# Performance work log

Measured on AMD Instinct MI355X. Metric: run time of the kernel, lower is better.

The kernel has to match this reference:

```python
import jax, jax.numpy as jnp
from jax import lax
import numpy as np

B, T, D, U = 32, 2048, 512, 512


def setup_inputs() -> dict:
    key = jax.random.key(0)
    k1, k2, k3 = jax.random.split(key, 3)
    x = jax.random.normal(k1, (B, T, D), dtype=jnp.float32)
    # keras 'uniform' initializer ~ U(-0.05, 0.05)
    kernel = jax.random.uniform(k2, (D, U), dtype=jnp.float32, minval=-0.05, maxval=0.05)
    recurrent_kernel = jax.random.uniform(k3, (U, U), dtype=jnp.float32, minval=-0.05, maxval=0.05)
    return {"x": x, "kernel": kernel, "recurrent_kernel": recurrent_kernel}


def reference(x, kernel, recurrent_kernel):
    # Linear RNN: h_t = x_t @ W + h_{t-1} @ U, h_0 = 0 (keras RNN default zero state).
    # Precompute the input projection as one big GEMM (same math, batched once).
    xk = jnp.einsum('btd,du->btu', x, kernel)  # [B, T, U]

    def step(h, xt):
        h = xt + h @ recurrent_kernel
        return h, h

    h0 = jnp.zeros((x.shape[0], recurrent_kernel.shape[0]), dtype=x.dtype)
    _, ys = lax.scan(step, h0, jnp.swapaxes(xk, 0, 1))  # ys: [T, B, U]
    return jnp.swapaxes(ys, 0, 1)  # [B, T, U] (return_sequences=True semantics)
```

## Files before the change

kernel.cpp:

```cpp
#include <hip/hip_runtime.h>
#include <hip/hip_bf16.h>


#define B_ 32
#define T_ 2048
#define D_ 512
#define U_ 512
#define C_ 8
#define P_ 256

typedef unsigned short u16;
typedef __attribute__((ext_vector_type(8))) short bf16x8;
typedef __attribute__((ext_vector_type(4))) float f32x4;

__device__ __forceinline__ float bf2f(u16 h) {
    union { unsigned u; float f; } v; v.u = ((unsigned)h) << 16; return v.f;
}
__device__ __forceinline__ u16 f2bf(float f) {
    union { float f; unsigned u; } v; v.f = f;
    unsigned x = v.u;
    unsigned r = x + 0x7fffu + ((x >> 16) & 1u);
    return (u16)(r >> 16);
}

__global__ void prep_kernel(const float* __restrict__ W, const float* __restrict__ R,
                            u16* __restrict__ Wt, u16* __restrict__ Rt, u16* __restrict__ Rb) {
    int idx = blockIdx.x * blockDim.x + threadIdx.x;
    int r = idx >> 9, c = idx & 511;
    float w = W[idx];
    float rv = R[idx];
    Wt[c * 512 + r] = f2bf(w);
    Rt[c * 512 + r] = f2bf(rv);
    Rb[idx] = f2bf(rv);
}

__global__ __launch_bounds__(256, 3) void gemmA_kernel(const float* __restrict__ x,
        const u16* __restrict__ Wt, u16* __restrict__ xk) {
    int bid = blockIdx.x;
    int mg = bid >> 2, ng = bid & 3;
    int m0 = mg * 128, n0 = ng * 128;
    int w = threadIdx.x >> 6, l = threadIdx.x & 63;
    int wm = (w >> 1) * 64, wn = (w & 1) * 64;
    int lane_m = l & 15, quad = l >> 4;

    f32x4 acc[4][4];
#pragma unroll
    for (int i = 0; i < 4; i++)
#pragma unroll
        for (int j = 0; j < 4; j++) acc[i][j] = (f32x4){0.f, 0.f, 0.f, 0.f};

    const float* xbase = x + (size_t)(m0 + wm + lane_m) * D_ + quad * 8;
    const u16* wbase = Wt + (size_t)(n0 + wn + lane_m) * D_ + quad * 8;

    for (int kk = 0; kk < 16; kk++) {
        bf16x8 af[4], bf[4];
#pragma unroll
        for (int mi = 0; mi < 4; mi++) {
            const float* p = xbase + (size_t)mi * 16 * D_ + kk * 32;
            float4 lo = *(const float4*)p;
            float4 hi = *(const float4*)(p + 4);
            bf16x8 t;
            t[0] = (short)f2bf(lo.x); t[1] = (short)f2bf(lo.y);
            t[2] = (short)f2bf(lo.z); t[3] = (short)f2bf(lo.w);
            t[4] = (short)f2bf(hi.x); t[5] = (short)f2bf(hi.y);
            t[6] = (short)f2bf(hi.z); t[7] = (short)f2bf(hi.w);
            af[mi] = t;
        }
#pragma unroll
        for (int ni = 0; ni < 4; ni++)
            bf[ni] = *(const bf16x8*)(wbase + (size_t)ni * 16 * D_ + kk * 32);
#pragma unroll
        for (int mi = 0; mi < 4; mi++)
#pragma unroll
            for (int ni = 0; ni < 4; ni++)
                acc[mi][ni] = __builtin_amdgcn_mfma_f32_16x16x32_bf16(af[mi], bf[ni], acc[mi][ni], 0, 0, 0);
    }
#pragma unroll
    for (int mi = 0; mi < 4; mi++)
#pragma unroll
        for (int ni = 0; ni < 4; ni++) {
            int col = n0 + wn + ni * 16 + lane_m;
#pragma unroll
            for (int i = 0; i < 4; i++) {
                int row = m0 + wm + mi * 16 + quad * 4 + i;
                xk[(size_t)row * U_ + col] = f2bf(acc[mi][ni][i]);
            }
        }
}

__global__ __launch_bounds__(512, 2) void pass1_kernel(
        const u16* __restrict__ xk, const u16* __restrict__ Rt,
        float* __restrict__ Lc,
        float* __restrict__ Eout) {
    __shared__ u16 H[B_][U_ + 8];
    int k = blockIdx.x;
    int t0 = k * C_;
    int tid = threadIdx.x;
    int w = tid >> 6, l = tid & 63;
    int lane_m = l & 15, quad = l >> 4;
    int wn = w * 64;

    for (int idx = tid; idx < B_ * U_; idx += 512) {
        int b = idx >> 9, u = idx & 511;
        H[b][u] = 0;
    }
    __syncthreads();

    f32x4 acc[2][4];
    for (int t = t0; t < t0 + C_; t++) {
#pragma unroll
        for (int mi = 0; mi < 2; mi++)
#pragma unroll
            for (int ni = 0; ni < 4; ni++) {
                int u = wn + ni * 16 + lane_m;
#pragma unroll
                for (int i = 0; i < 4; i++) {
                    int b = mi * 16 + quad * 4 + i;
                    acc[mi][ni][i] = bf2f(xk[((size_t)b * T_ + t) * U_ + u]);
                }
            }
        for (int kk = 0; kk < 16; kk++) {
            bf16x8 a0 = *(const bf16x8*)&H[lane_m][kk * 32 + quad * 8];
            bf16x8 a1 = *(const bf16x8*)&H[16 + lane_m][kk * 32 + quad * 8];
#pragma unroll
            for (int ni = 0; ni < 4; ni++) {
                bf16x8 b = *(const bf16x8*)(Rt + (size_t)(wn + ni * 16 + lane_m) * U_ + kk * 32 + quad * 8);
                acc[0][ni] = __builtin_amdgcn_mfma_f32_16x16x32_bf16(a0, b, acc[0][ni], 0, 0, 0);
                acc[1][ni] = __builtin_amdgcn_mfma_f32_16x16x32_bf16(a1, b, acc[1][ni], 0, 0, 0);
            }
        }
        __syncthreads();
#pragma unroll
        for (int mi = 0; mi < 2; mi++)
#pragma unroll
            for (int ni = 0; ni < 4; ni++) {
                int u = wn + ni * 16 + lane_m;
#pragma unroll
                for (int i = 0; i < 4; i++) {
                    int b = mi * 16 + quad * 4 + i;
                    float v = acc[mi][ni][i];
                    H[b][u] = f2bf(v);
                    Lc[((size_t)t * B_ + b) * U_ + u] = v;
                }
            }
        __syncthreads();
    }
#pragma unroll
    for (int mi = 0; mi < 2; mi++)
#pragma unroll
        for (int ni = 0; ni < 4; ni++) {
            int u = wn + ni * 16 + lane_m;
#pragma unroll
            for (int i = 0; i < 4; i++) {
                int b = mi * 16 + quad * 4 + i;
                Eout[((size_t)k * B_ + b) * U_ + u] = acc[mi][ni][i];
            }
        }
}

__global__ __launch_bounds__(512, 2) void ks_kernel(const float* __restrict__ Esrc,
        float* __restrict__ Edst, const u16* __restrict__ Mt, int d) {
    int k = blockIdx.x;
    int tid = threadIdx.x, w = tid >> 6, l = tid & 63;
    if (k < d) {
        const float4* s = (const float4*)(Esrc + (size_t)k * B_ * U_);
        float4* dst = (float4*)(Edst + (size_t)k * B_ * U_);
        for (int i = tid; i < B_ * U_ / 4; i += 512) dst[i] = s[i];
        return;
    }
    int lane_m = l & 15, quad = l >> 4, wn = w * 64;
    const float* Ek = Esrc + (size_t)k * B_ * U_;
    const float* Ep = Esrc + (size_t)(k - d) * B_ * U_;
    f32x4 acc[2][4];
#pragma unroll
    for (int mi = 0; mi < 2; mi++)
#pragma unroll
        for (int ni = 0; ni < 4; ni++) {
            int u = wn + ni * 16 + lane_m;
#pragma unroll
            for (int i = 0; i < 4; i++) {
                int b = mi * 16 + quad * 4 + i;
                acc[mi][ni][i] = Ek[(size_t)b * U_ + u];
            }
        }
    for (int kk = 0; kk < 16; kk++) {
        bf16x8 a[2];
#pragma unroll
        for (int mi = 0; mi < 2; mi++) {
            const float* p = Ep + (size_t)(mi * 16 + lane_m) * U_ + kk * 32 + quad * 8;
            float4 lo = *(const float4*)p;
            float4 hi = *(const float4*)(p + 4);
            bf16x8 t;
            t[0] = (short)f2bf(lo.x); t[1] = (short)f2bf(lo.y);
            t[2] = (short)f2bf(lo.z); t[3] = (short)f2bf(lo.w);
            t[4] = (short)f2bf(hi.x); t[5] = (short)f2bf(hi.y);
            t[6] = (short)f2bf(hi.z); t[7] = (short)f2bf(hi.w);
            a[mi] = t;
        }
#pragma unroll
        for (int ni = 0; ni < 4; ni++) {
            bf16x8 b = *(const bf16x8*)(Mt + (size_t)(wn + ni * 16 + lane_m) * U_ + kk * 32 + quad * 8);
            acc[0][ni] = __builtin_amdgcn_mfma_f32_16x16x32_bf16(a[0], b, acc[0][ni], 0, 0, 0);
            acc[1][ni] = __builtin_amdgcn_mfma_f32_16x16x32_bf16(a[1], b, acc[1][ni], 0, 0, 0);
        }
    }
#pragma unroll
    for (int mi = 0; mi < 2; mi++)
#pragma unroll
        for (int ni = 0; ni < 4; ni++) {
            int u = wn + ni * 16 + lane_m;
#pragma unroll
            for (int i = 0; i < 4; i++) {
                int b = mi * 16 + quad * 4 + i;
                Edst[(size_t)k * B_ * U_ + (size_t)b * U_ + u] = acc[mi][ni][i];
            }
        }
}

__global__ __launch_bounds__(512, 2) void carry_kernel(const float* __restrict__ Eb,
        const u16* __restrict__ Rt, u16* __restrict__ Sb, u16* __restrict__ S2) {
    int k = blockIdx.x;
    int tid = threadIdx.x, w = tid >> 6, l = tid & 63;
    if (k == P_ - 1) {
        for (int i = tid; i < B_ * U_; i += 512) { Sb[i] = 0; S2[i] = 0; }
        return;
    }
    const float* E = Eb + (size_t)k * B_ * U_;
    u16* sb = Sb + (size_t)(k + 1) * B_ * U_;
    u16* s2o = S2 + (size_t)(k + 1) * B_ * U_;
    for (int i = tid; i < B_ * U_; i += 512) sb[i] = f2bf(E[i]);

    int lane_m = l & 15, quad = l >> 4, wn = w * 64;
    f32x4 acc[2][4];
#pragma unroll
    for (int mi = 0; mi < 2; mi++)
#pragma unroll
        for (int ni = 0; ni < 4; ni++) acc[mi][ni] = (f32x4){0.f, 0.f, 0.f, 0.f};
    for (int kk = 0; kk < 16; kk++) {
        bf16x8 a[2];
#pragma unroll
        for (int mi = 0; mi < 2; mi++) {
            const float* p = E + (size_t)(mi * 16 + lane_m) * U_ + kk * 32 + quad * 8;
            float4 lo = *(const float4*)p;
            float4 hi = *(const float4*)(p + 4);
            bf16x8 t;
            t[0] = (short)f2bf(lo.x); t[1] = (short)f2bf(lo.y);
            t[2] = (short)f2bf(lo.z); t[3] = (short)f2bf(lo.w);
            t[4] = (short)f2bf(hi.x); t[5] = (short)f2bf(hi.y);
            t[6] = (short)f2bf(hi.z); t[7] = (short)f2bf(hi.w);
            a[mi] = t;
        }
#pragma unroll
        for (int ni = 0; ni < 4; ni++) {
            bf16x8 b = *(const bf16x8*)(Rt + (size_t)(wn + ni * 16 + lane_m) * U_ + kk * 32 + quad * 8);
            acc[0][ni] = __builtin_amdgcn_mfma_f32_16x16x32_bf16(a[0], b, acc[0][ni], 0, 0, 0);
            acc[1][ni] = __builtin_amdgcn_mfma_f32_16x16x32_bf16(a[1], b, acc[1][ni], 0, 0, 0);
        }
    }
#pragma unroll
    for (int mi = 0; mi < 2; mi++)
#pragma unroll
        for (int ni = 0; ni < 4; ni++) {
            int u = wn + ni * 16 + lane_m;
#pragma unroll
            for (int i = 0; i < 4; i++) {
                int b = mi * 16 + quad * 4 + i;
                s2o[(size_t)b * U_ + u] = f2bf(acc[mi][ni][i]);
            }
        }
}

__global__ __launch_bounds__(256, 2) void pass3g_kernel(
        const float* __restrict__ Lc, const u16* __restrict__ Sb,
        const u16* __restrict__ S2,
        const u16* __restrict__ P2, const u16* __restrict__ P4,
        const u16* __restrict__ P6, const u16* __restrict__ P8,
        float* __restrict__ out) {
    int bid = blockIdx.x;
    int k = bid >> 3, j = bid & 7;
    int t = k * C_ + j;
    int tid = threadIdx.x, w = tid >> 6, l = tid & 63;
    int lane_m = l & 15, quad = l >> 4;
    int wn = w * 128;

    f32x4 acc[2][8];
    const float* lc = Lc + (size_t)t * B_ * U_;
#pragma unroll
    for (int mi = 0; mi < 2; mi++)
#pragma unroll
        for (int ni = 0; ni < 8; ni++) {
            int u = wn + ni * 16 + lane_m;
#pragma unroll
            for (int i = 0; i < 4; i++) {
                int b = mi * 16 + quad * 4 + i;
                acc[mi][ni][i] = lc[(size_t)b * U_ + u];
            }
        }

    if (j == 0) {
        const u16* s2 = S2 + (size_t)k * B_ * U_;
#pragma unroll
        for (int mi = 0; mi < 2; mi++)
#pragma unroll
            for (int ni = 0; ni < 8; ni++) {
                int u = wn + ni * 16 + lane_m;
#pragma unroll
                for (int i = 0; i < 4; i++) {
                    int b = mi * 16 + quad * 4 + i;
                    acc[mi][ni][i] += bf2f(s2[(size_t)b * U_ + u]);
                }
            }
    } else {
        const u16* A = ((j & 1) ? Sb : S2) + (size_t)k * B_ * U_;
        const u16* Bm = (j & 1)
            ? ((j == 1) ? P2 : (j == 3) ? P4 : (j == 5) ? P6 : P8)
            : ((j == 2) ? P2 : (j == 4) ? P4 : P6);
        for (int kk = 0; kk < 16; kk++) {
            bf16x8 a0 = *(const bf16x8*)(A + (size_t)lane_m * U_ + kk * 32 + quad * 8);
            bf16x8 a1 = *(const bf16x8*)(A + (size_t)(16 + lane_m) * U_ + kk * 32 + quad * 8);
#pragma unroll
            for (int ni = 0; ni < 8; ni++) {
                bf16x8 bv = *(const bf16x8*)(Bm + (size_t)(wn + ni * 16 + lane_m) * U_ + kk * 32 + quad * 8);
                acc[0][ni] = __builtin_amdgcn_mfma_f32_16x16x32_bf16(a0, bv, acc[0][ni], 0, 0, 0);
                acc[1][ni] = __builtin_amdgcn_mfma_f32_16x16x32_bf16(a1, bv, acc[1][ni], 0, 0, 0);
            }
        }
    }

#pragma unroll
    for (int mi = 0; mi < 2; mi++)
#pragma unroll
        for (int ni = 0; ni < 8; ni++) {
            int u = wn + ni * 16 + lane_m;
#pragma unroll
            for (int i = 0; i < 4; i++) {
                int b = mi * 16 + quad * 4 + i;
                out[((size_t)b * T_ + t) * U_ + u] = acc[mi][ni][i];
            }
        }
}

__global__ __launch_bounds__(256, 3) void matsq_kernel(const u16* __restrict__ Arm,
        const u16* __restrict__ Bcm, u16* __restrict__ Zrm, u16* __restrict__ Zcm) {
    int bid = blockIdx.x;
    int mg = bid >> 1, cg = bid & 1;
    int m0 = mg * 32, n0 = cg * 256;
    int tid = threadIdx.x, w = tid >> 6, l = tid & 63;
    int lane_m = l & 15, quad = l >> 4;
    int wn = n0 + w * 64;
    f32x4 acc[2][4];
#pragma unroll
    for (int mi = 0; mi < 2; mi++)
#pragma unroll
        for (int ni = 0; ni < 4; ni++) acc[mi][ni] = (f32x4){0.f, 0.f, 0.f, 0.f};
    for (int kk = 0; kk < 16; kk++) {
        bf16x8 a0 = *(const bf16x8*)(Arm + (size_t)(m0 + lane_m) * 512 + kk * 32 + quad * 8);
        bf16x8 a1 = *(const bf16x8*)(Arm + (size_t)(m0 + 16 + lane_m) * 512 + kk * 32 + quad * 8);
#pragma unroll
        for (int ni = 0; ni < 4; ni++) {
            bf16x8 b = *(const bf16x8*)(Bcm + (size_t)(wn + ni * 16 + lane_m) * 512 + kk * 32 + quad * 8);
            acc[0][ni] = __builtin_amdgcn_mfma_f32_16x16x32_bf16(a0, b, acc[0][ni], 0, 0, 0);
            acc[1][ni] = __builtin_amdgcn_mfma_f32_16x16x32_bf16(a1, b, acc[1][ni], 0, 0, 0);
        }
    }
#pragma unroll
    for (int mi = 0; mi < 2; mi++)
#pragma unroll
        for (int ni = 0; ni < 4; ni++) {
            int col = wn + ni * 16 + lane_m;
#pragma unroll
            for (int i = 0; i < 4; i++) {
                int row = m0 + mi * 16 + quad * 4 + i;
                u16 v = f2bf(acc[mi][ni][i]);
                Zrm[(size_t)row * 512 + col] = v;
                Zcm[(size_t)col * 512 + row] = v;
            }
        }
}

extern "C" void kernel_launch(void* const* d_in, const int* in_sizes, int n_in,
                              void* d_out, int out_size, void* d_ws, size_t ws_size,
                              hipStream_t stream) {
    const float* x = (const float*)d_in[0];
    const float* W = (const float*)d_in[1];
    const float* R = (const float*)d_in[2];
    float* out = (float*)d_out;

    char* ws = (char*)d_ws;
    u16* xk = (u16*)ws;                ws += (size_t)B_ * T_ * U_ * 2;
    float* Lc = (float*)ws;            ws += (size_t)B_ * T_ * U_ * 4;
    float* Ea = (float*)ws;            ws += (size_t)P_ * B_ * U_ * 4;
    float* Eb = (float*)ws;            ws += (size_t)P_ * B_ * U_ * 4;
    u16* Sb = (u16*)ws;                ws += (size_t)P_ * B_ * U_ * 2;
    u16* S2 = (u16*)ws;                ws += (size_t)P_ * B_ * U_ * 2;
    const size_t MSZ = (size_t)512 * 512 * 2;
    u16* Wt = (u16*)ws;  ws += MSZ;
    u16* Rt = (u16*)ws;  ws += MSZ;
    u16* Rb = (u16*)ws;  ws += MSZ;
    u16* Prm[6]; u16* Pcm[6];
    Prm[0] = Rt; Pcm[0] = Rb;
    for (int i = 1; i <= 5; i++) { Prm[i] = (u16*)ws; ws += MSZ; Pcm[i] = (u16*)ws; ws += MSZ; }
    u16* P6rm = (u16*)ws; ws += MSZ;
    u16* P6cm = (u16*)ws; ws += MSZ;

    prep_kernel<<<1024, 256, 0, stream>>>(W, R, Wt, Rt, Rb);
    matsq_kernel<<<32, 256, 0, stream>>>(Prm[0], Pcm[0], Prm[1], Pcm[1]);
    matsq_kernel<<<32, 256, 0, stream>>>(Prm[1], Pcm[1], Prm[2], Pcm[2]);
    matsq_kernel<<<32, 256, 0, stream>>>(Prm[2], Pcm[1], P6rm, P6cm);
    matsq_kernel<<<32, 256, 0, stream>>>(Prm[2], Pcm[2], Prm[3], Pcm[3]);
    matsq_kernel<<<32, 256, 0, stream>>>(Prm[3], Pcm[3], Prm[4], Pcm[4]);
    matsq_kernel<<<32, 256, 0, stream>>>(Prm[4], Pcm[4], Prm[5], Pcm[5]);

    gemmA_kernel<<<2048, 256, 0, stream>>>(x, Wt, xk);
    pass1_kernel<<<P_, 512, 0, stream>>>(xk, Rt, Lc, Ea);
    ks_kernel<<<P_, 512, 0, stream>>>(Ea, Eb, Prm[3], 1);
    ks_kernel<<<P_, 512, 0, stream>>>(Eb, Ea, Prm[4], 2);
    ks_kernel<<<P_, 512, 0, stream>>>(Ea, Eb, Prm[5], 4);
    carry_kernel<<<P_, 512, 0, stream>>>(Eb, Rt, Sb, S2);
    pass3g_kernel<<<P_ * C_, 256, 0, stream>>>(Lc, Sb, S2, Prm[1], Prm[2], P6rm, Prm[3], out);
}
```

Measured before the change: 872.3 us.

## Pre-convert x to bf16, transpose xk/Lc layouts, double-buffer pass1 state, keep bf16 carries

Adds a standalone kernel that converts x to bf16 once, so the input GEMM reads bf16 directly, and raises its occupancy hint. xk is stored time-major and Lc batch-innermost so pass1 and pass3 can use contiguous vector loads and stores. pass1 double-buffers the hidden state in shared memory, which removes one barrier per step, skips the first matmul while h is zero, and prefetches the next xk step into registers. The scan and carry kernels now also emit bf16 copies so later stages skip fp32-to-bf16 conversion, at the cost of extra buffers and a separate conversion pass over x.

```diff
diff --git a/kernel.cpp b/kernel.cpp
--- a/kernel.cpp
+++ b/kernel.cpp
@@ -34,7 +34,23 @@
     Rb[idx] = f2bf(rv);
 }
 
-__global__ __launch_bounds__(256, 3) void gemmA_kernel(const float* __restrict__ x,
+__global__ __launch_bounds__(256) void xcvt_kernel(const float* __restrict__ x,
+                                                   u16* __restrict__ xb) {
+    const size_t n8 = (size_t)B_ * T_ * D_ / 8;
+    size_t stride = (size_t)gridDim.x * blockDim.x;
+    for (size_t i = (size_t)blockIdx.x * blockDim.x + threadIdx.x; i < n8; i += stride) {
+        const float4* p = (const float4*)(x + i * 8);
+        float4 lo = p[0], hi = p[1];
+        bf16x8 t;
+        t[0] = (short)f2bf(lo.x); t[1] = (short)f2bf(lo.y);
+        t[2] = (short)f2bf(lo.z); t[3] = (short)f2bf(lo.w);
+        t[4] = (short)f2bf(hi.x); t[5] = (short)f2bf(hi.y);
+        t[6] = (short)f2bf(hi.z); t[7] = (short)f2bf(hi.w);
+        *(bf16x8*)(xb + i * 8) = t;
+    }
+}
+
+__global__ __launch_bounds__(256, 4) void gemmA_kernel(const u16* __restrict__ xb,
         const u16* __restrict__ Wt, u16* __restrict__ xk) {
     int bid = blockIdx.x;
     int mg = bid >> 2, ng = bid & 3;
@@ -49,26 +65,17 @@
 #pragma unroll
         for (int j = 0; j < 4; j++) acc[i][j] = (f32x4){0.f, 0.f, 0.f, 0.f};
 
-    const float* xbase = x + (size_t)(m0 + wm + lane_m) * D_ + quad * 8;
-    const u16* wbase = Wt + (size_t)(n0 + wn + lane_m) * D_ + quad * 8;
+    const u16* abase = xb + (size_t)(m0 + wm + lane_m) * D_ + quad * 8;
+    const u16* bbase = Wt + (size_t)(n0 + wn + lane_m) * D_ + quad * 8;
 
     for (int kk = 0; kk < 16; kk++) {
         bf16x8 af[4], bf[4];
 #pragma unroll
-        for (int mi = 0; mi < 4; mi++) {
-            const float* p = xbase + (size_t)mi * 16 * D_ + kk * 32;
-            float4 lo = *(const float4*)p;
-            float4 hi = *(const float4*)(p + 4);
-            bf16x8 t;
-            t[0] = (short)f2bf(lo.x); t[1] = (short)f2bf(lo.y);
-            t[2] = (short)f2bf(lo.z); t[3] = (short)f2bf(lo.w);
-            t[4] = (short)f2bf(hi.x); t[5] = (short)f2bf(hi.y);
-            t[6] = (short)f2bf(hi.z); t[7] = (short)f2bf(hi.w);
-            af[mi] = t;
-        }
+        for (int mi = 0; mi < 4; mi++)
+            af[mi] = *(const bf16x8*)(abase + (size_t)mi * 16 * D_ + kk * 32);
 #pragma unroll
         for (int ni = 0; ni < 4; ni++)
-            bf[ni] = *(const bf16x8*)(wbase + (size_t)ni * 16 * D_ + kk * 32);
+            bf[ni] = *(const bf16x8*)(bbase + (size_t)ni * 16 * D_ + kk * 32);
 #pragma unroll
         for (int mi = 0; mi < 4; mi++)
 #pragma unroll
@@ -83,16 +90,18 @@
 #pragma unroll
             for (int i = 0; i < 4; i++) {
                 int row = m0 + wm + mi * 16 + quad * 4 + i;
-                xk[(size_t)row * U_ + col] = f2bf(acc[mi][ni][i]);
-            }
-        }
-}
-
-__global__ __launch_bounds__(512, 2) void pass1_kernel(
+                int t = row & 2047, b = row >> 11;
+                xk[(((size_t)t * 32 + b) << 9) + col] = f2bf(acc[mi][ni][i]);
+            }
+        }
+}
+
+__global__ __launch_bounds__(512) void pass1_kernel(
         const u16* __restrict__ xk, const u16* __restrict__ Rt,
         float* __restrict__ Lc,
-        float* __restrict__ Eout) {
-    __shared__ u16 H[B_][U_ + 8];
+        float* __restrict__ Eout,
+        u16* __restrict__ Ebf) {
+    __shared__ u16 H[2][B_][U_ + 8];
     int k = blockIdx.x;
     int t0 = k * C_;
     int tid = threadIdx.x;
@@ -100,14 +109,8 @@
     int lane_m = l & 15, quad = l >> 4;
     int wn = w * 64;
 
-    for (int idx = tid; idx < B_ * U_; idx += 512) {
-        int b = idx >> 9, u = idx & 511;
-        H[b][u] = 0;
-    }
-    __syncthreads();
-
-    f32x4 acc[2][4];
-    for (int t = t0; t < t0 + C_; t++) {
+    u16 xc[2][4][4], xn[2][4][4];
+    auto loadx = [&](u16 (&d)[2][4][4], int t) {
 #pragma unroll
         for (int mi = 0; mi < 2; mi++)
 #pragma unroll
@@ -116,34 +119,60 @@
 #pragma unroll
                 for (int i = 0; i < 4; i++) {
                     int b = mi * 16 + quad * 4 + i;
-                    acc[mi][ni][i] = bf2f(xk[((size_t)b * T_ + t) * U_ + u]);
+                    d[mi][ni][i] = xk[(((size_t)t * 32 + b) << 9) + u];
                 }
             }
-        for (int kk = 0; kk < 16; kk++) {
-            bf16x8 a0 = *(const bf16x8*)&H[lane_m][kk * 32 + quad * 8];
-            bf16x8 a1 = *(const bf16x8*)&H[16 + lane_m][kk * 32 + quad * 8];
-#pragma unroll
-            for (int ni = 0; ni < 4; ni++) {
-                bf16x8 b = *(const bf16x8*)(Rt + (size_t)(wn + ni * 16 + lane_m) * U_ + kk * 32 + quad * 8);
-                acc[0][ni] = __builtin_amdgcn_mfma_f32_16x16x32_bf16(a0, b, acc[0][ni], 0, 0, 0);
-                acc[1][ni] = __builtin_amdgcn_mfma_f32_16x16x32_bf16(a1, b, acc[1][ni], 0, 0, 0);
-            }
-        }
-        __syncthreads();
+    };
+    loadx(xc, t0);
+
+    f32x4 acc[2][4];
+    int cur = 0;
+#pragma unroll
+    for (int j = 0; j < C_; j++) {
+        int t = t0 + j;
+        if (j + 1 < C_) loadx(xn, t + 1);
+#pragma unroll
+        for (int mi = 0; mi < 2; mi++)
+#pragma unroll
+            for (int ni = 0; ni < 4; ni++)
+#pragma unroll
+                for (int i = 0; i < 4; i++)
+                    acc[mi][ni][i] = bf2f(xc[mi][ni][i]);
+        if (j > 0) {
+            for (int kk = 0; kk < 16; kk++) {
+                bf16x8 a0 = *(const bf16x8*)&H[cur][lane_m][kk * 32 + quad * 8];
+                bf16x8 a1 = *(const bf16x8*)&H[cur][16 + lane_m][kk * 32 + quad * 8];
+#pragma unroll
+                for (int ni = 0; ni < 4; ni++) {
+                    bf16x8 b = *(const bf16x8*)(Rt + (size_t)(wn + ni * 16 + lane_m) * U_ + kk * 32 + quad * 8);
+                    acc[0][ni] = __builtin_amdgcn_mfma_f32_16x16x32_bf16(a0, b, acc[0][ni], 0, 0, 0);
+                    acc[1][ni] = __builtin_amdgcn_mfma_f32_16x16x32_bf16(a1, b, acc[1][ni], 0, 0, 0);
+                }
+            }
+        }
 #pragma unroll
         for (int mi = 0; mi < 2; mi++)
 #pragma unroll
             for (int ni = 0; ni < 4; ni++) {
                 int u = wn + ni * 16 + lane_m;
-#pragma unroll
-                for (int i = 0; i < 4; i++) {
-                    int b = mi * 16 + quad * 4 + i;
-                    float v = acc[mi][ni][i];
-                    H[b][u] = f2bf(v);
-                    Lc[((size_t)t * B_ + b) * U_ + u] = v;
-                }
+                int b0 = mi * 16 + quad * 4;
+                f32x4 v = acc[mi][ni];
+                *(f32x4*)(Lc + ((size_t)t * 512 + u) * 32 + b0) = v;
+#pragma unroll
+                for (int i = 0; i < 4; i++)
+                    H[cur ^ 1][b0 + i][u] = f2bf(v[i]);
             }
         __syncthreads();
+        cur ^= 1;
+        if (j + 1 < C_) {
+#pragma unroll
+            for (int mi = 0; mi < 2; mi++)
+#pragma unroll
+                for (int ni = 0; ni < 4; ni++)
+#pragma unroll
+                    for (int i = 0; i < 4; i++)
+                        xc[mi][ni][i] = xn[mi][ni][i];
+        }
     }
 #pragma unroll
     for (int mi = 0; mi < 2; mi++)
@@ -153,24 +182,31 @@
 #pragma unroll
             for (int i = 0; i < 4; i++) {
                 int b = mi * 16 + quad * 4 + i;
-                Eout[((size_t)k * B_ + b) * U_ + u] = acc[mi][ni][i];
+                float v = acc[mi][ni][i];
+                Eout[((size_t)k * B_ + b) * U_ + u] = v;
+                Ebf[((size_t)k * B_ + b) * U_ + u] = f2bf(v);
             }
         }
 }
 
 __global__ __launch_bounds__(512, 2) void ks_kernel(const float* __restrict__ Esrc,
-        float* __restrict__ Edst, const u16* __restrict__ Mt, int d) {
+        const u16* __restrict__ Esrcbf,
+        float* __restrict__ Edst, u16* __restrict__ Edstbf,
+        const u16* __restrict__ Mt, int d) {
     int k = blockIdx.x;
     int tid = threadIdx.x, w = tid >> 6, l = tid & 63;
     if (k < d) {
         const float4* s = (const float4*)(Esrc + (size_t)k * B_ * U_);
         float4* dst = (float4*)(Edst + (size_t)k * B_ * U_);
         for (int i = tid; i < B_ * U_ / 4; i += 512) dst[i] = s[i];
+        const uint4* sb = (const uint4*)(Esrcbf + (size_t)k * B_ * U_);
+        uint4* db = (uint4*)(Edstbf + (size_t)k * B_ * U_);
+        for (int i = tid; i < B_ * U_ / 8; i += 512) db[i] = sb[i];
         return;
     }
     int lane_m = l & 15, quad = l >> 4, wn = w * 64;
     const float* Ek = Esrc + (size_t)k * B_ * U_;
-    const float* Ep = Esrc + (size_t)(k - d) * B_ * U_;
+    const u16* Epb = Esrcbf + (size_t)(k - d) * B_ * U_;
     f32x4 acc[2][4];
 #pragma unroll
     for (int mi = 0; mi < 2; mi++)
@@ -184,24 +220,13 @@
             }
         }
     for (int kk = 0; kk < 16; kk++) {
-        bf16x8 a[2];
-#pragma unroll
-        for (int mi = 0; mi < 2; mi++) {
-            const float* p = Ep + (size_t)(mi * 16 + lane_m) * U_ + kk * 32 + quad * 8;
-            float4 lo = *(const float4*)p;
-            float4 hi = *(const float4*)(p + 4);
-            bf16x8 t;
-            t[0] = (short)f2bf(lo.x); t[1] = (short)f2bf(lo.y);
-            t[2] = (short)f2bf(lo.z); t[3] = (short)f2bf(lo.w);
-            t[4] = (short)f2bf(hi.x); t[5] = (short)f2bf(hi.y);
-            t[6] = (short)f2bf(hi.z); t[7] = (short)f2bf(hi.w);
-            a[mi] = t;
-        }
+        bf16x8 a0 = *(const bf16x8*)(Epb + (size_t)lane_m * U_ + kk * 32 + quad * 8);
+        bf16x8 a1 = *(const bf16x8*)(Epb + (size_t)(16 + lane_m) * U_ + kk * 32 + quad * 8);
 #pragma unroll
         for (int ni = 0; ni < 4; ni++) {
             bf16x8 b = *(const bf16x8*)(Mt + (size_t)(wn + ni * 16 + lane_m) * U_ + kk * 32 + quad * 8);
-            acc[0][ni] = __builtin_amdgcn_mfma_f32_16x16x32_bf16(a[0], b, acc[0][ni], 0, 0, 0);
-            acc[1][ni] = __builtin_amdgcn_mfma_f32_16x16x32_bf16(a[1], b, acc[1][ni], 0, 0, 0);
+            acc[0][ni] = __builtin_amdgcn_mfma_f32_16x16x32_bf16(a0, b, acc[0][ni], 0, 0, 0);
+            acc[1][ni] = __builtin_amdgcn_mfma_f32_16x16x32_bf16(a1, b, acc[1][ni], 0, 0, 0);
         }
     }
 #pragma unroll
@@ -212,12 +237,15 @@
 #pragma unroll
             for (int i = 0; i < 4; i++) {
                 int b = mi * 16 + quad * 4 + i;
-                Edst[(size_t)k * B_ * U_ + (size_t)b * U_ + u] = acc[mi][ni][i];
-            }
-        }
-}
-
-__global__ __launch_bounds__(512, 2) void carry_kernel(const float* __restrict__ Eb,
+                float v = acc[mi][ni][i];
+                size_t o = (size_t)k * B_ * U_ + (size_t)b * U_ + u;
+                Edst[o] = v;
+                Edstbf[o] = f2bf(v);
+            }
+        }
+}
+
+__global__ __launch_bounds__(512, 2) void carry_kernel(const u16* __restrict__ Ebf,
         const u16* __restrict__ Rt, u16* __restrict__ Sb, u16* __restrict__ S2) {
     int k = blockIdx.x;
     int tid = threadIdx.x, w = tid >> 6, l = tid & 63;
@@ -225,11 +253,14 @@
         for (int i = tid; i < B_ * U_; i += 512) { Sb[i] = 0; S2[i] = 0; }
         return;
     }
-    const float* E = Eb + (size_t)k * B_ * U_;
+    const u16* E = Ebf + (size_t)k * B_ * U_;
     u16* sb = Sb + (size_t)(k + 1) * B_ * U_;
     u16* s2o = S2 + (size_t)(k + 1) * B_ * U_;
-    for (int i = tid; i < B_ * U_; i += 512) sb[i] = f2bf(E[i]);
-
+    {
+        const uint4* s = (const uint4*)E;
+        uint4* dv = (uint4*)sb;
+        for (int i = tid; i < B_ * U_ / 8; i += 512) dv[i] = s[i];
+    }
     int lane_m = l & 15, quad = l >> 4, wn = w * 64;
     f32x4 acc[2][4];
 #pragma unroll
@@ -237,24 +268,13 @@
 #pragma unroll
         for (int ni = 0; ni < 4; ni++) acc[mi][ni] = (f32x4){0.f, 0.f, 0.f, 0.f};
     for (int kk = 0; kk < 16; kk++) {
-        bf16x8 a[2];
-#pragma unroll
-        for (int mi = 0; mi < 2; mi++) {
-            const float* p = E + (size_t)(mi * 16 + lane_m) * U_ + kk * 32 + quad * 8;
-            float4 lo = *(const float4*)p;
-            float4 hi = *(const float4*)(p + 4);
-            bf16x8 t;
-            t[0] = (short)f2bf(lo.x); t[1] = (short)f2bf(lo.y);
-            t[2] = (short)f2bf(lo.z); t[3] = (short)f2bf(lo.w);
-            t[4] = (short)f2bf(hi.x); t[5] = (short)f2bf(hi.y);
-            t[6] = (short)f2bf(hi.z); t[7] = (short)f2bf(hi.w);
-            a[mi] = t;
-        }
+        bf16x8 a0 = *(const bf16x8*)(E + (size_t)lane_m * U_ + kk * 32 + quad * 8);
+        bf16x8 a1 = *(const bf16x8*)(E + (size_t)(16 + lane_m) * U_ + kk * 32 + quad * 8);
 #pragma unroll
         for (int ni = 0; ni < 4; ni++) {
             bf16x8 b = *(const bf16x8*)(Rt + (size_t)(wn + ni * 16 + lane_m) * U_ + kk * 32 + quad * 8);
-            acc[0][ni] = __builtin_amdgcn_mfma_f32_16x16x32_bf16(a[0], b, acc[0][ni], 0, 0, 0);
-            acc[1][ni] = __builtin_amdgcn_mfma_f32_16x16x32_bf16(a[1], b, acc[1][ni], 0, 0, 0);
+            acc[0][ni] = __builtin_amdgcn_mfma_f32_16x16x32_bf16(a0, b, acc[0][ni], 0, 0, 0);
+            acc[1][ni] = __builtin_amdgcn_mfma_f32_16x16x32_bf16(a1, b, acc[1][ni], 0, 0, 0);
         }
     }
 #pragma unroll
@@ -290,11 +310,8 @@
 #pragma unroll
         for (int ni = 0; ni < 8; ni++) {
             int u = wn + ni * 16 + lane_m;
-#pragma unroll
-            for (int i = 0; i < 4; i++) {
-                int b = mi * 16 + quad * 4 + i;
-                acc[mi][ni][i] = lc[(size_t)b * U_ + u];
-            }
+            int b0 = mi * 16 + quad * 4;
+            acc[mi][ni] = *(const f32x4*)(lc + (size_t)u * 32 + b0);
         }
 
     if (j == 0) {
@@ -389,8 +406,11 @@
     char* ws = (char*)d_ws;
     u16* xk = (u16*)ws;                ws += (size_t)B_ * T_ * U_ * 2;
     float* Lc = (float*)ws;            ws += (size_t)B_ * T_ * U_ * 4;
+    u16* xb = (u16*)Lc;
     float* Ea = (float*)ws;            ws += (size_t)P_ * B_ * U_ * 4;
     float* Eb = (float*)ws;            ws += (size_t)P_ * B_ * U_ * 4;
+    u16* Eabf = (u16*)ws;              ws += (size_t)P_ * B_ * U_ * 2;
+    u16* Ebbf = (u16*)ws;              ws += (size_t)P_ * B_ * U_ * 2;
     u16* Sb = (u16*)ws;                ws += (size_t)P_ * B_ * U_ * 2;
     u16* S2 = (u16*)ws;                ws += (size_t)P_ * B_ * U_ * 2;
     const size_t MSZ = (size_t)512 * 512 * 2;
@@ -411,11 +431,12 @@
     matsq_kernel<<<32, 256, 0, stream>>>(Prm[3], Pcm[3], Prm[4], Pcm[4]);
     matsq_kernel<<<32, 256, 0, stream>>>(Prm[4], Pcm[4], Prm[5], Pcm[5]);
 
-    gemmA_kernel<<<2048, 256, 0, stream>>>(x, Wt, xk);
-    pass1_kernel<<<P_, 512, 0, stream>>>(xk, Rt, Lc, Ea);
-    ks_kernel<<<P_, 512, 0, stream>>>(Ea, Eb, Prm[3], 1);
-    ks_kernel<<<P_, 512, 0, stream>>>(Eb, Ea, Prm[4], 2);
-    ks_kernel<<<P_, 512, 0, stream>>>(Ea, Eb, Prm[5], 4);
-    carry_kernel<<<P_, 512, 0, stream>>>(Eb, Rt, Sb, S2);
+    xcvt_kernel<<<2048, 256, 0, stream>>>(x, xb);
+    gemmA_kernel<<<2048, 256, 0, stream>>>(xb, Wt, xk);
+    pass1_kernel<<<P_, 512, 0, stream>>>(xk, Rt, Lc, Ea, Eabf);
+    ks_kernel<<<P_, 512, 0, stream>>>(Ea, Eabf, Eb, Ebbf, Prm[3], 1);
+    ks_kernel<<<P_, 512, 0, stream>>>(Eb, Ebbf, Ea, Eabf, Prm[4], 2);
+    ks_kernel<<<P_, 512, 0, stream>>>(Ea, Eabf, Eb, Ebbf, Prm[5], 4);
+    carry_kernel<<<P_, 512, 0, stream>>>(Ebbf, Rt, Sb, S2);
     pass3g_kernel<<<P_ * C_, 256, 0, stream>>>(Lc, Sb, S2, Prm[1], Prm[2], P6rm, Prm[3], out);
 }
```

After: 864.7 us. About the same (-0.9%).
